# Kernel optimization log

Measured on AMD Instinct MI355X. Metric: run time of the kernel, lower is better.

The kernel has to match this reference:

```python
import jax, jax.numpy as jnp
import numpy as np

# Model config (matches init_kwargs)
DIM = 2048
INTER = 1408          # moe_inter_dim
E = 16                # n_routed_experts
TOPK = 4              # n_activated_experts
G = 4                 # n_expert_groups
TOPK_G = 2            # n_limited_groups
N_SHARED = 2
SHARED_INTER = N_SHARED * INTER  # 2816
ROUTE_SCALE = 1.0


def setup_inputs() -> dict:
    key = jax.random.key(0)
    ks = jax.random.split(key, 8)
    s = 0.02
    x = jax.random.normal(ks[0], (1, 2048, DIM), dtype=jnp.float32)
    Wg = jax.random.normal(ks[1], (E, DIM), dtype=jnp.float32) * s      # gate weight
    W1 = jax.random.normal(ks[2], (E, INTER, DIM), dtype=jnp.float32) * s  # expert gate proj
    W3 = jax.random.normal(ks[3], (E, INTER, DIM), dtype=jnp.float32) * s  # expert up proj
    W2 = jax.random.normal(ks[4], (E, DIM, INTER), dtype=jnp.float32) * s  # expert down proj
    Ws1 = jax.random.normal(ks[5], (SHARED_INTER, DIM), dtype=jnp.float32) * s
    Ws3 = jax.random.normal(ks[6], (SHARED_INTER, DIM), dtype=jnp.float32) * s
    Ws2 = jax.random.normal(ks[7], (DIM, SHARED_INTER), dtype=jnp.float32) * s
    return {"x": x, "Wg": Wg, "W1": W1, "W3": W3, "W2": W2,
            "Ws1": Ws1, "Ws3": Ws3, "Ws2": Ws2}


def _moe_forward(x, Wg, W1, W3, W2, Ws1, Ws3, Ws2):
    B, S, D = x.shape
    xt = x.reshape(-1, D)              # [T, D]
    T = xt.shape[0]

    # ---- Gate: group-limited top-k routing (bias is None since dim != 7168) ----
    scores = jax.nn.softmax(xt @ Wg.T, axis=-1)          # [T, E]
    sg = scores.reshape(T, G, E // G)                    # [T, G, E/G]
    group_scores = sg.max(axis=-1)                       # amax per group
    gidx = jax.lax.top_k(group_scores, TOPK_G)[1]        # [T, TOPK_G]
    gmask = jax.nn.one_hot(gidx, G, dtype=jnp.float32).sum(axis=1) > 0  # [T, G] kept groups
    masked = jnp.where(gmask[:, :, None], sg, -jnp.inf).reshape(T, E)
    topi = jax.lax.top_k(masked, TOPK)[1]                # [T, TOPK] expert indices
    weights = jnp.take_along_axis(scores, topi, axis=1) * ROUTE_SCALE  # original_scores gather

    # ---- Routed experts: dense per-expert SwiGLU FFN, zero-weight combine ----
    # combine[t, e] = sum over k of weights[t, k] * (topi[t, k] == e)
    combine = jnp.zeros((T, E), xt.dtype).at[jnp.arange(T)[:, None], topi].add(weights)
    h = jax.nn.silu(jnp.einsum('td,eid->eti', xt, W1)) * jnp.einsum('td,eid->eti', xt, W3)
    expert_out = jnp.einsum('eti,edi->etd', h, W2)       # [E, T, D]
    y = jnp.einsum('etd,te->td', expert_out, combine)    # [T, D]

    # ---- Shared expert (applied to all tokens) ----
    z = (jax.nn.silu(xt @ Ws1.T) * (xt @ Ws3.T)) @ Ws2.T

    return (y + z).reshape(B, S, D)


def reference(x, Wg, W1, W3, W2, Ws1, Ws3, Ws2):
    return _moe_forward(x, Wg, W1, W3, W2, Ws1, Ws3, Ws2)
```

## Files before the change

kernel.cpp:

```cpp
#include <hip/hip_runtime.h>
#include <stdint.h>

#define D_MODEL  2048
#define N_INTER  1408
#define SH_INTER 2816
#define T_TOK    2048
#define NSLOT    (T_TOK * 4)

typedef __attribute__((ext_vector_type(8))) short bf16x8;
typedef __attribute__((ext_vector_type(4))) float f32x4;

__device__ __forceinline__ unsigned short f2bf(float f){
  unsigned int b = __builtin_bit_cast(unsigned int, f);
  b = (b + 0x7FFFu + ((b >> 16) & 1u)) >> 16;
  return (unsigned short)b;
}
__device__ __forceinline__ float bf2f(unsigned short h){
  unsigned int b = ((unsigned int)h) << 16;
  return __builtin_bit_cast(float, b);
}

#define GLOAD16(gp, lp) __builtin_amdgcn_global_load_lds( \
    (const __attribute__((address_space(1))) unsigned int*)(gp), \
    (__attribute__((address_space(3))) unsigned int*)(lp), 16, 0, 0)

__global__ void cvt_bf16_kernel(const float* __restrict__ x,
                                unsigned short* __restrict__ o, int n4){
  const int stride = gridDim.x * blockDim.x;
  for (int i = blockIdx.x * blockDim.x + threadIdx.x; i < n4; i += stride){
    const float4 v = ((const float4*)x)[i];
    ushort4 u; u.x = f2bf(v.x); u.y = f2bf(v.y); u.z = f2bf(v.z); u.w = f2bf(v.w);
    ((ushort4*)o)[i] = u;
  }
}

__global__ void gate_kernel(const float* __restrict__ x, const float* __restrict__ Wg,
                            int* __restrict__ cnt, int* __restrict__ list,
                            float* __restrict__ wslot){
  const int t = blockIdx.x;
  const int l = threadIdx.x;
  const int e = l & 15, q = l >> 4;
  const float* xr = x + (size_t)t * D_MODEL + q * 512;
  const float* wr = Wg + (size_t)e * D_MODEL + q * 512;
  float p = 0.f;
  #pragma unroll 4
  for (int i = 0; i < 512; i += 4){
    float4 xv = *(const float4*)(xr + i);
    float4 wv = *(const float4*)(wr + i);
    p += xv.x*wv.x + xv.y*wv.y + xv.z*wv.z + xv.w*wv.w;
  }
  p += __shfl_xor(p, 16);
  p += __shfl_xor(p, 32);
  float mx = p;
  for (int d = 1; d < 16; d <<= 1) mx = fmaxf(mx, __shfl_xor(mx, d));
  float ex = __expf(p - mx);
  float sum = ex;
  for (int d = 1; d < 16; d <<= 1) sum += __shfl_xor(sum, d);
  const float sc = ex / sum;
  float gm = fmaxf(sc, __shfl_xor(sc, 1));
  gm = fmaxf(gm, __shfl_xor(gm, 2));
  const float g0 = __shfl(gm, 0), g1 = __shfl(gm, 4),
              g2 = __shfl(gm, 8), g3 = __shfl(gm, 12);
  const int grp = e >> 2;
  const float gs[4] = {g0, g1, g2, g3};
  int grank = 0;
  #pragma unroll
  for (int j = 0; j < 4; ++j)
    if (gs[j] > gm || (gs[j] == gm && j < grp)) grank++;
  const float msc = (grank < 2) ? sc : -INFINITY;
  int erank = 0;
  #pragma unroll
  for (int j = 0; j < 16; ++j){
    const float oj = __shfl(msc, j);
    if (oj > msc || (oj == msc && j < e)) erank++;
  }
  if (q == 0 && erank < 4 && msc > -INFINITY){
    const int pos = atomicAdd(&cnt[e], 1);
    const int slot = (t << 2) | erank;
    list[e * T_TOK + pos] = slot;
    wslot[slot] = sc;
  }
}

template<int MODE>
__global__ __launch_bounds__(256, 2)
void gemm4_kernel(const unsigned short* __restrict__ A,
                  const unsigned short* __restrict__ B,
                  void* __restrict__ OutP,
                  const int* __restrict__ list,
                  const int* __restrict__ cnt,
                  int N, int K, int MT, int NT)
{
  constexpr bool GATHER = (MODE >= 2);
  __shared__ unsigned short As[2 * 128 * 32];
  __shared__ unsigned short Bs[2 * 128 * 32];

  const int per = gridDim.x >> 3;
  const int gsw = (blockIdx.x & 7) * per + (blockIdx.x >> 3);
  const int mt   = gsw % MT;
  const int rest = gsw / MT;
  const int nt = GATHER ? (rest % NT) : rest;
  const int e  = GATHER ? (rest / NT) : 0;

  const int cntE = GATHER ? cnt[e] : (MT * 128);
  if (mt * 128 >= cntE) return;

  const int tid = threadIdx.x, wid = tid >> 6, lane = tid & 63;

  const int rt0 = 32 * wid + (lane >> 2), rt1 = rt0 + 16;
  const int sx0 = ((lane & 3) ^ ((rt0 >> 1) & 3)) << 3;
  const int sx1 = ((lane & 3) ^ ((rt1 >> 1) & 3)) << 3;

  int ar0, ar1;
  if constexpr (GATHER){
    const int lim = cntE - 1;
    int p0 = mt * 128 + rt0; p0 = p0 < lim ? p0 : lim;
    int p1 = mt * 128 + rt1; p1 = p1 < lim ? p1 : lim;
    const int e0 = list[e * T_TOK + p0], e1 = list[e * T_TOK + p1];
    ar0 = (MODE == 2) ? (e0 >> 2) : e0;
    ar1 = (MODE == 2) ? (e1 >> 2) : e1;
  } else { ar0 = mt * 128 + rt0; ar1 = mt * 128 + rt1; }

  const unsigned short* pa0 = A + (size_t)ar0 * K + sx0;
  const unsigned short* pa1 = A + (size_t)ar1 * K + sx1;
  const size_t Boff = GATHER ? (size_t)e * N * K : 0;
  const unsigned short* pb0 = B + Boff + (size_t)(nt * 128 + rt0) * K + sx0;
  const unsigned short* pb1 = B + Boff + (size_t)(nt * 128 + rt1) * K + sx1;

  const int aW0 = (32 * wid) * 32, aW1 = (32 * wid + 16) * 32;
  const int bufStride = 128 * 32;

  const int wr = wid >> 1, wc = wid & 1, lr = lane & 15, lq = lane >> 4;
  const int fx = ((lq ^ ((lr >> 1) & 3)) << 3);
  int aoff[4], boff[4];
  #pragma unroll
  for (int m = 0; m < 4; ++m) aoff[m] = (wr * 64 + m * 16 + lr) * 32 + fx;
  #pragma unroll
  for (int n = 0; n < 4; ++n) boff[n] = (wc * 64 + n * 16 + lr) * 32 + fx;

  f32x4 acc[4][4];
  const f32x4 zero = {0.f, 0.f, 0.f, 0.f};
  #pragma unroll
  for (int m = 0; m < 4; ++m)
    #pragma unroll
    for (int n = 0; n < 4; ++n) acc[m][n] = zero;

  const int KT = K >> 5;
  GLOAD16(pa0, As + aW0);
  GLOAD16(pa1, As + aW1);
  GLOAD16(pb0, Bs + aW0);
  GLOAD16(pb1, Bs + aW1);
  pa0 += 32; pa1 += 32; pb0 += 32; pb1 += 32;
  int cur = 0;

  for (int kt = 0; kt < KT; ++kt){
    __syncthreads();
    if (kt + 1 < KT){
      const int nx = cur ^ 1;
      GLOAD16(pa0, As + nx * bufStride + aW0);
      GLOAD16(pa1, As + nx * bufStride + aW1);
      GLOAD16(pb0, Bs + nx * bufStride + aW0);
      GLOAD16(pb1, Bs + nx * bufStride + aW1);
      pa0 += 32; pa1 += 32; pb0 += 32; pb1 += 32;
    }
    const unsigned short* aC = As + cur * bufStride;
    const unsigned short* bC = Bs + cur * bufStride;
    bf16x8 af[4];
    #pragma unroll
    for (int m = 0; m < 4; ++m) af[m] = *(const bf16x8*)(aC + aoff[m]);
    #pragma unroll
    for (int n = 0; n < 4; ++n){
      const bf16x8 bfr = *(const bf16x8*)(bC + boff[n]);
      #pragma unroll
      for (int m = 0; m < 4; ++m)
        acc[m][n] = __builtin_amdgcn_mfma_f32_16x16x32_bf16(af[m], bfr, acc[m][n], 0, 0, 0);
    }
    cur ^= 1;
  }

  const int colBase = nt * 128 + wc * 64;
  #pragma unroll
  for (int m = 0; m < 4; ++m){
    #pragma unroll
    for (int r = 0; r < 4; ++r){
      const int grow = mt * 128 + wr * 64 + m * 16 + lq * 4 + r;
      if constexpr (MODE == 1){
        float* op = (float*)OutP + (size_t)grow * N + colBase;
        #pragma unroll
        for (int n = 0; n < 4; ++n) op[n * 16 + lr] = acc[m][n][r];
      } else if constexpr (MODE == 0){
        unsigned short* op = (unsigned short*)OutP + (size_t)grow * N + colBase;
        #pragma unroll
        for (int n = 0; n < 4; ++n) op[n * 16 + lr] = f2bf(acc[m][n][r]);
      } else {
        if (grow >= cntE) continue;
        const int orow = list[e * T_TOK + grow];
        unsigned short* op = (unsigned short*)OutP + (size_t)orow * N + colBase;
        #pragma unroll
        for (int n = 0; n < 4; ++n) op[n * 16 + lr] = f2bf(acc[m][n][r]);
      }
    }
  }
}

__global__ void swiglu_kernel(unsigned short* __restrict__ G,
                              const unsigned short* __restrict__ U, int n8){
  const int stride = gridDim.x * blockDim.x;
  for (int i = blockIdx.x * blockDim.x + threadIdx.x; i < n8; i += stride){
    const bf16x8 g = ((const bf16x8*)G)[i];
    const bf16x8 u = ((const bf16x8*)U)[i];
    bf16x8 h;
    #pragma unroll
    for (int j = 0; j < 8; ++j){
      const float gv = bf2f((unsigned short)g[j]);
      const float uv = bf2f((unsigned short)u[j]);
      h[j] = (short)f2bf(gv / (1.f + __expf(-gv)) * uv);
    }
    ((bf16x8*)G)[i] = h;
  }
}

__global__ void combine_kernel(const unsigned short* __restrict__ H2,
                               const float* __restrict__ wslot,
                               float* __restrict__ out){
  const int t = blockIdx.x;
  const int c = threadIdx.x * 8;
  float w[4];
  #pragma unroll
  for (int k = 0; k < 4; ++k) w[k] = wslot[t * 4 + k];
  float* o = out + (size_t)t * D_MODEL + c;
  float a[8];
  #pragma unroll
  for (int j = 0; j < 8; ++j) a[j] = o[j];
  #pragma unroll
  for (int k = 0; k < 4; ++k){
    const bf16x8 hv = *(const bf16x8*)(H2 + (size_t)(t * 4 + k) * D_MODEL + c);
    #pragma unroll
    for (int j = 0; j < 8; ++j) a[j] += w[k] * bf2f((unsigned short)hv[j]);
  }
  #pragma unroll
  for (int j = 0; j < 8; ++j) o[j] = a[j];
}

extern "C" void kernel_launch(void* const* d_in, const int* in_sizes, int n_in,
                              void* d_out, int out_size, void* d_ws, size_t ws_size,
                              hipStream_t stream)
{
  const float* x   = (const float*)d_in[0];
  const float* Wg  = (const float*)d_in[1];
  const float* W1  = (const float*)d_in[2];
  const float* W3  = (const float*)d_in[3];
  const float* W2  = (const float*)d_in[4];
  const float* Ws1 = (const float*)d_in[5];
  const float* Ws3 = (const float*)d_in[6];
  const float* Ws2 = (const float*)d_in[7];
  float* out = (float*)d_out;

  char* ws = (char*)d_ws;
  int*   cnt   = (int*)(ws);
  int*   list  = (int*)(ws + 4096);
  float* wslot = (float*)(ws + 4096 + 131072);
  unsigned short* xbf  = (unsigned short*)(ws + ((size_t)1   << 20));
  unsigned short* H2   = (unsigned short*)(ws + ((size_t)1   << 20));
  unsigned short* Ubuf = (unsigned short*)(ws + ((size_t)10  << 20));
  unsigned short* Wb   = (unsigned short*)(ws + ((size_t)34  << 20));
  unsigned short* Gbuf = (unsigned short*)(ws + ((size_t)123 << 20));
  unsigned short* Wb2  = Wb + (size_t)SH_INTER * D_MODEL;

  hipMemsetAsync(cnt, 0, 4096, stream);
  cvt_bf16_kernel<<<2048, 256, 0, stream>>>(x, xbf, T_TOK * D_MODEL / 4);
  gate_kernel<<<T_TOK, 64, 0, stream>>>(x, Wg, cnt, list, wslot);

  cvt_bf16_kernel<<<4096, 256, 0, stream>>>(Ws1, Wb,  SH_INTER * D_MODEL / 4);
  cvt_bf16_kernel<<<4096, 256, 0, stream>>>(Ws3, Wb2, SH_INTER * D_MODEL / 4);
  gemm4_kernel<0><<<16 * 22, 256, 0, stream>>>(xbf, Wb,  Gbuf, nullptr, nullptr,
                                               SH_INTER, D_MODEL, 16, 22);
  gemm4_kernel<0><<<16 * 22, 256, 0, stream>>>(xbf, Wb2, Ubuf, nullptr, nullptr,
                                               SH_INTER, D_MODEL, 16, 22);
  swiglu_kernel<<<2048, 256, 0, stream>>>(Gbuf, Ubuf, T_TOK * SH_INTER / 8);
  cvt_bf16_kernel<<<4096, 256, 0, stream>>>(Ws2, Wb, D_MODEL * SH_INTER / 4);
  gemm4_kernel<1><<<16 * 16, 256, 0, stream>>>(Gbuf, Wb, out, nullptr, nullptr,
                                               D_MODEL, SH_INTER, 16, 16);

  cvt_bf16_kernel<<<8192, 256, 0, stream>>>(W1, Wb, 16 * N_INTER * D_MODEL / 4);
  gemm4_kernel<2><<<16 * 11 * 16, 256, 0, stream>>>(xbf, Wb, Gbuf, list, cnt,
                                                    N_INTER, D_MODEL, 16, 11);
  cvt_bf16_kernel<<<8192, 256, 0, stream>>>(W3, Wb, 16 * N_INTER * D_MODEL / 4);
  gemm4_kernel<2><<<16 * 11 * 16, 256, 0, stream>>>(xbf, Wb, Ubuf, list, cnt,
                                                    N_INTER, D_MODEL, 16, 11);
  swiglu_kernel<<<2048, 256, 0, stream>>>(Gbuf, Ubuf, NSLOT * N_INTER / 8);
  cvt_bf16_kernel<<<8192, 256, 0, stream>>>(W2, Wb, 16 * D_MODEL * N_INTER / 4);
  gemm4_kernel<3><<<16 * 16 * 16, 256, 0, stream>>>(Gbuf, Wb, H2, list, cnt,
                                                    D_MODEL, N_INTER, 16, 16);
  combine_kernel<<<T_TOK, 256, 0, stream>>>(H2, wslot, out);
}
```

Before: 670.8 us.

## Fuse fp32 weight conversion into GEMM loads, merge gate/up GEMMs, split-K shared down

Drops the separate fp32-to-bf16 weight conversion passes. The GEMM now loads fp32 weights straight into LDS and converts each fragment to bf16 in registers before the MFMA. The gate and up projections run as one launch over a concatenated N range, with swiglu reading the interleaved output. The shared down-projection uses a 2-way split-K whose partials are summed in the combine kernel. This removes about 4 passes over the weights, but it doubles B-tile LDS traffic and puts conversion ALU work into the inner loop.

Result: slower. 711.6 us (+6.1%).

```diff
diff --git a/kernel.cpp b/kernel.cpp
--- a/kernel.cpp
+++ b/kernel.cpp
@@ -1,4 +1,5 @@
 #include <hip/hip_runtime.h>
+#include <hip/hip_bf16.h>
 #include <stdint.h>
 
 #define D_MODEL  2048
@@ -14,6 +15,10 @@
   unsigned int b = __builtin_bit_cast(unsigned int, f);
   b = (b + 0x7FFFu + ((b >> 16) & 1u)) >> 16;
   return (unsigned short)b;
+}
+__device__ __forceinline__ unsigned short f2bfh(float f){
+  __hip_bfloat16 h = __float2bfloat16(f);
+  return __builtin_bit_cast(unsigned short, h);
 }
 __device__ __forceinline__ float bf2f(unsigned short h){
   unsigned int b = ((unsigned int)h) << 16;
@@ -82,35 +87,43 @@
   }
 }
 
-template<int MODE>
-__global__ __launch_bounds__(256, 2)
-void gemm4_kernel(const unsigned short* __restrict__ A,
-                  const unsigned short* __restrict__ B,
+template<int MODE, int NTH, int KSPLIT>
+__global__ __launch_bounds__(256, 3)
+void gemm5_kernel(const unsigned short* __restrict__ A,
+                  const float* __restrict__ B1,
+                  const float* __restrict__ B3,
                   void* __restrict__ OutP,
                   const int* __restrict__ list,
                   const int* __restrict__ cnt,
-                  int N, int K, int MT, int NT)
+                  int N, int K, int MT, int NTtot, size_t eStride)
 {
   constexpr bool GATHER = (MODE >= 2);
   __shared__ unsigned short As[2 * 128 * 32];
-  __shared__ unsigned short Bs[2 * 128 * 32];
+  __shared__ float          Bs[2 * 128 * 32];
 
   const int per = gridDim.x >> 3;
   const int gsw = (blockIdx.x & 7) * per + (blockIdx.x >> 3);
-  const int mt   = gsw % MT;
-  const int rest = gsw / MT;
-  const int nt = GATHER ? (rest % NT) : rest;
-  const int e  = GATHER ? (rest / NT) : 0;
+  const int mt = gsw % MT;
+  int r1 = gsw / MT;
+  int ks = 0;
+  if constexpr (KSPLIT > 1){ ks = r1 % KSPLIT; r1 /= KSPLIT; }
+  const int nt = GATHER ? (r1 % NTtot) : r1;
+  const int e  = GATHER ? (r1 / NTtot) : 0;
 
   const int cntE = GATHER ? cnt[e] : (MT * 128);
   if (mt * 128 >= cntE) return;
 
+  const float* Bsel; int ntb;
+  if constexpr (NTH > 0){
+    if (nt >= NTH){ Bsel = B3; ntb = nt - NTH; } else { Bsel = B1; ntb = nt; }
+  } else { Bsel = B1; ntb = nt; }
+  if constexpr (GATHER) Bsel += (size_t)e * eStride;
+
   const int tid = threadIdx.x, wid = tid >> 6, lane = tid & 63;
+  const int kOff = ks * (K / KSPLIT);
 
   const int rt0 = 32 * wid + (lane >> 2), rt1 = rt0 + 16;
-  const int sx0 = ((lane & 3) ^ ((rt0 >> 1) & 3)) << 3;
-  const int sx1 = ((lane & 3) ^ ((rt1 >> 1) & 3)) << 3;
-
+  const int sxA = ((lane & 3) ^ ((lane >> 3) & 3)) << 3;
   int ar0, ar1;
   if constexpr (GATHER){
     const int lim = cntE - 1;
@@ -120,23 +133,32 @@
     ar0 = (MODE == 2) ? (e0 >> 2) : e0;
     ar1 = (MODE == 2) ? (e1 >> 2) : e1;
   } else { ar0 = mt * 128 + rt0; ar1 = mt * 128 + rt1; }
-
-  const unsigned short* pa0 = A + (size_t)ar0 * K + sx0;
-  const unsigned short* pa1 = A + (size_t)ar1 * K + sx1;
-  const size_t Boff = GATHER ? (size_t)e * N * K : 0;
-  const unsigned short* pb0 = B + Boff + (size_t)(nt * 128 + rt0) * K + sx0;
-  const unsigned short* pb1 = B + Boff + (size_t)(nt * 128 + rt1) * K + sx1;
-
-  const int aW0 = (32 * wid) * 32, aW1 = (32 * wid + 16) * 32;
-  const int bufStride = 128 * 32;
+  const unsigned short* pa0 = A + (size_t)ar0 * K + kOff + sxA;
+  const unsigned short* pa1 = A + (size_t)ar1 * K + kOff + sxA;
+  const int aW0 = (32 * wid) * 32, aW1 = aW0 + 16 * 32;
+  const int aStride = 128 * 32;
+
+  const int brt = 32 * wid + (lane >> 3);
+  const int sxB = ((lane & 7) ^ ((lane >> 3) & 7)) << 2;
+  const float* pb0 = Bsel + (size_t)(ntb * 128 + brt     ) * K + kOff + sxB;
+  const float* pb1 = Bsel + (size_t)(ntb * 128 + brt +  8) * K + kOff + sxB;
+  const float* pb2 = Bsel + (size_t)(ntb * 128 + brt + 16) * K + kOff + sxB;
+  const float* pb3 = Bsel + (size_t)(ntb * 128 + brt + 24) * K + kOff + sxB;
+  const int bW0 = wid * 1024, bW1 = bW0 + 256, bW2 = bW0 + 512, bW3 = bW0 + 768;
+  const int bStride = 128 * 32;
 
   const int wr = wid >> 1, wc = wid & 1, lr = lane & 15, lq = lane >> 4;
-  const int fx = ((lq ^ ((lr >> 1) & 3)) << 3);
-  int aoff[4], boff[4];
-  #pragma unroll
-  for (int m = 0; m < 4; ++m) aoff[m] = (wr * 64 + m * 16 + lr) * 32 + fx;
-  #pragma unroll
-  for (int n = 0; n < 4; ++n) boff[n] = (wc * 64 + n * 16 + lr) * 32 + fx;
+  const int fxA = ((lq ^ ((lr >> 1) & 3)) << 3);
+  int aoff[4], boff0[4], boff1[4];
+  #pragma unroll
+  for (int m = 0; m < 4; ++m) aoff[m] = (wr * 64 + m * 16 + lr) * 32 + fxA;
+  #pragma unroll
+  for (int n = 0; n < 4; ++n){
+    const int rowB = wc * 64 + n * 16 + lr;
+    const int ph0 = (2 * lq) ^ (lr & 7);
+    boff0[n] = rowB * 32 + ph0 * 4;
+    boff1[n] = rowB * 32 + (ph0 ^ 1) * 4;
+  }
 
   f32x4 acc[4][4];
   const f32x4 zero = {0.f, 0.f, 0.f, 0.f};
@@ -145,32 +167,42 @@
     #pragma unroll
     for (int n = 0; n < 4; ++n) acc[m][n] = zero;
 
-  const int KT = K >> 5;
+  const int KTL = (K >> 5) / KSPLIT;
   GLOAD16(pa0, As + aW0);
   GLOAD16(pa1, As + aW1);
-  GLOAD16(pb0, Bs + aW0);
-  GLOAD16(pb1, Bs + aW1);
-  pa0 += 32; pa1 += 32; pb0 += 32; pb1 += 32;
+  GLOAD16(pb0, Bs + bW0);
+  GLOAD16(pb1, Bs + bW1);
+  GLOAD16(pb2, Bs + bW2);
+  GLOAD16(pb3, Bs + bW3);
+  pa0 += 32; pa1 += 32; pb0 += 32; pb1 += 32; pb2 += 32; pb3 += 32;
   int cur = 0;
 
-  for (int kt = 0; kt < KT; ++kt){
+  for (int kt = 0; kt < KTL; ++kt){
     __syncthreads();
-    if (kt + 1 < KT){
+    if (kt + 1 < KTL){
       const int nx = cur ^ 1;
-      GLOAD16(pa0, As + nx * bufStride + aW0);
-      GLOAD16(pa1, As + nx * bufStride + aW1);
-      GLOAD16(pb0, Bs + nx * bufStride + aW0);
-      GLOAD16(pb1, Bs + nx * bufStride + aW1);
-      pa0 += 32; pa1 += 32; pb0 += 32; pb1 += 32;
+      GLOAD16(pa0, As + nx * aStride + aW0);
+      GLOAD16(pa1, As + nx * aStride + aW1);
+      GLOAD16(pb0, Bs + nx * bStride + bW0);
+      GLOAD16(pb1, Bs + nx * bStride + bW1);
+      GLOAD16(pb2, Bs + nx * bStride + bW2);
+      GLOAD16(pb3, Bs + nx * bStride + bW3);
+      pa0 += 32; pa1 += 32; pb0 += 32; pb1 += 32; pb2 += 32; pb3 += 32;
     }
-    const unsigned short* aC = As + cur * bufStride;
-    const unsigned short* bC = Bs + cur * bufStride;
+    const unsigned short* aC = As + cur * aStride;
+    const float* bC = Bs + cur * bStride;
     bf16x8 af[4];
     #pragma unroll
     for (int m = 0; m < 4; ++m) af[m] = *(const bf16x8*)(aC + aoff[m]);
     #pragma unroll
     for (int n = 0; n < 4; ++n){
-      const bf16x8 bfr = *(const bf16x8*)(bC + boff[n]);
+      const f32x4 v0 = *(const f32x4*)(bC + boff0[n]);
+      const f32x4 v1 = *(const f32x4*)(bC + boff1[n]);
+      bf16x8 bfr;
+      bfr[0] = (short)f2bfh(v0[0]); bfr[1] = (short)f2bfh(v0[1]);
+      bfr[2] = (short)f2bfh(v0[2]); bfr[3] = (short)f2bfh(v0[3]);
+      bfr[4] = (short)f2bfh(v1[0]); bfr[5] = (short)f2bfh(v1[1]);
+      bfr[6] = (short)f2bfh(v1[2]); bfr[7] = (short)f2bfh(v1[3]);
       #pragma unroll
       for (int m = 0; m < 4; ++m)
         acc[m][n] = __builtin_amdgcn_mfma_f32_16x16x32_bf16(af[m], bfr, acc[m][n], 0, 0, 0);
@@ -185,7 +217,7 @@
     for (int r = 0; r < 4; ++r){
       const int grow = mt * 128 + wr * 64 + m * 16 + lq * 4 + r;
       if constexpr (MODE == 1){
-        float* op = (float*)OutP + (size_t)grow * N + colBase;
+        float* op = (float*)OutP + (size_t)ks * MT * 128 * N + (size_t)grow * N + colBase;
         #pragma unroll
         for (int n = 0; n < 4; ++n) op[n * 16 + lr] = acc[m][n][r];
       } else if constexpr (MODE == 0){
@@ -203,12 +235,14 @@
   }
 }
 
-__global__ void swiglu_kernel(unsigned short* __restrict__ G,
-                              const unsigned short* __restrict__ U, int n8){
+__global__ void swiglu_split_kernel(const unsigned short* __restrict__ GU,
+                                    unsigned short* __restrict__ H,
+                                    int n8, int NI8){
   const int stride = gridDim.x * blockDim.x;
   for (int i = blockIdx.x * blockDim.x + threadIdx.x; i < n8; i += stride){
-    const bf16x8 g = ((const bf16x8*)G)[i];
-    const bf16x8 u = ((const bf16x8*)U)[i];
+    const int r = i / NI8, c = i - r * NI8;
+    const bf16x8 g = ((const bf16x8*)GU)[(size_t)r * 2 * NI8 + c];
+    const bf16x8 u = ((const bf16x8*)GU)[(size_t)r * 2 * NI8 + NI8 + c];
     bf16x8 h;
     #pragma unroll
     for (int j = 0; j < 8; ++j){
@@ -216,11 +250,12 @@
       const float uv = bf2f((unsigned short)u[j]);
       h[j] = (short)f2bf(gv / (1.f + __expf(-gv)) * uv);
     }
-    ((bf16x8*)G)[i] = h;
+    ((bf16x8*)H)[i] = h;
   }
 }
 
 __global__ void combine_kernel(const unsigned short* __restrict__ H2,
+                               const float* __restrict__ P,
                                const float* __restrict__ wslot,
                                float* __restrict__ out){
   const int t = blockIdx.x;
@@ -228,16 +263,18 @@
   float w[4];
   #pragma unroll
   for (int k = 0; k < 4; ++k) w[k] = wslot[t * 4 + k];
-  float* o = out + (size_t)t * D_MODEL + c;
+  const float* p0 = P + (size_t)t * D_MODEL + c;
+  const float* p1 = P + (size_t)(T_TOK + t) * D_MODEL + c;
   float a[8];
   #pragma unroll
-  for (int j = 0; j < 8; ++j) a[j] = o[j];
+  for (int j = 0; j < 8; ++j) a[j] = p0[j] + p1[j];
   #pragma unroll
   for (int k = 0; k < 4; ++k){
     const bf16x8 hv = *(const bf16x8*)(H2 + (size_t)(t * 4 + k) * D_MODEL + c);
     #pragma unroll
     for (int j = 0; j < 8; ++j) a[j] += w[k] * bf2f((unsigned short)hv[j]);
   }
+  float* o = out + (size_t)t * D_MODEL + c;
   #pragma unroll
   for (int j = 0; j < 8; ++j) o[j] = a[j];
 }
@@ -261,36 +298,32 @@
   int*   list  = (int*)(ws + 4096);
   float* wslot = (float*)(ws + 4096 + 131072);
   unsigned short* xbf  = (unsigned short*)(ws + ((size_t)1   << 20));
-  unsigned short* H2   = (unsigned short*)(ws + ((size_t)1   << 20));
-  unsigned short* Ubuf = (unsigned short*)(ws + ((size_t)10  << 20));
-  unsigned short* Wb   = (unsigned short*)(ws + ((size_t)34  << 20));
-  unsigned short* Gbuf = (unsigned short*)(ws + ((size_t)123 << 20));
-  unsigned short* Wb2  = Wb + (size_t)SH_INTER * D_MODEL;
+  unsigned short* GU_s = (unsigned short*)(ws + ((size_t)10  << 20));
+  unsigned short* Hs   = (unsigned short*)(ws + ((size_t)34  << 20));
+  unsigned short* GU_r = (unsigned short*)(ws + ((size_t)46  << 20));
+  unsigned short* Hc   = (unsigned short*)(ws + ((size_t)93  << 20));
+  unsigned short* H2   = (unsigned short*)(ws + ((size_t)10  << 20));
+  float*          P    = (float*)        (ws + ((size_t)117 << 20));
 
   hipMemsetAsync(cnt, 0, 4096, stream);
   cvt_bf16_kernel<<<2048, 256, 0, stream>>>(x, xbf, T_TOK * D_MODEL / 4);
   gate_kernel<<<T_TOK, 64, 0, stream>>>(x, Wg, cnt, list, wslot);
 
-  cvt_bf16_kernel<<<4096, 256, 0, stream>>>(Ws1, Wb,  SH_INTER * D_MODEL / 4);
-  cvt_bf16_kernel<<<4096, 256, 0, stream>>>(Ws3, Wb2, SH_INTER * D_MODEL / 4);
-  gemm4_kernel<0><<<16 * 22, 256, 0, stream>>>(xbf, Wb,  Gbuf, nullptr, nullptr,
-                                               SH_INTER, D_MODEL, 16, 22);
-  gemm4_kernel<0><<<16 * 22, 256, 0, stream>>>(xbf, Wb2, Ubuf, nullptr, nullptr,
-                                               SH_INTER, D_MODEL, 16, 22);
-  swiglu_kernel<<<2048, 256, 0, stream>>>(Gbuf, Ubuf, T_TOK * SH_INTER / 8);
-  cvt_bf16_kernel<<<4096, 256, 0, stream>>>(Ws2, Wb, D_MODEL * SH_INTER / 4);
-  gemm4_kernel<1><<<16 * 16, 256, 0, stream>>>(Gbuf, Wb, out, nullptr, nullptr,
-                                               D_MODEL, SH_INTER, 16, 16);
-
-  cvt_bf16_kernel<<<8192, 256, 0, stream>>>(W1, Wb, 16 * N_INTER * D_MODEL / 4);
-  gemm4_kernel<2><<<16 * 11 * 16, 256, 0, stream>>>(xbf, Wb, Gbuf, list, cnt,
-                                                    N_INTER, D_MODEL, 16, 11);
-  cvt_bf16_kernel<<<8192, 256, 0, stream>>>(W3, Wb, 16 * N_INTER * D_MODEL / 4);
-  gemm4_kernel<2><<<16 * 11 * 16, 256, 0, stream>>>(xbf, Wb, Ubuf, list, cnt,
-                                                    N_INTER, D_MODEL, 16, 11);
-  swiglu_kernel<<<2048, 256, 0, stream>>>(Gbuf, Ubuf, NSLOT * N_INTER / 8);
-  cvt_bf16_kernel<<<8192, 256, 0, stream>>>(W2, Wb, 16 * D_MODEL * N_INTER / 4);
-  gemm4_kernel<3><<<16 * 16 * 16, 256, 0, stream>>>(Gbuf, Wb, H2, list, cnt,
-                                                    D_MODEL, N_INTER, 16, 16);
-  combine_kernel<<<T_TOK, 256, 0, stream>>>(H2, wslot, out);
-}
+  gemm5_kernel<0, 22, 1><<<16 * 44, 256, 0, stream>>>(
+      xbf, Ws1, Ws3, GU_s, nullptr, nullptr, 2 * SH_INTER, D_MODEL, 16, 44, 0);
+  swiglu_split_kernel<<<2048, 256, 0, stream>>>(GU_s, Hs, T_TOK * SH_INTER / 8, SH_INTER / 8);
+
+  gemm5_kernel<1, 0, 2><<<16 * 16 * 2, 256, 0, stream>>>(
+      Hs, Ws2, nullptr, P, nullptr, nullptr, D_MODEL, SH_INTER, 16, 16, 0);
+
+  gemm5_kernel<2, 11, 1><<<16 * 22 * 16, 256, 0, stream>>>(
+      xbf, W1, W3, GU_r, list, cnt, 2 * N_INTER, D_MODEL, 16, 22,
+      (size_t)N_INTER * D_MODEL);
+  swiglu_split_kernel<<<2048, 256, 0, stream>>>(GU_r, Hc, NSLOT * N_INTER / 8, N_INTER / 8);
+
+  gemm5_kernel<3, 0, 1><<<16 * 16 * 16, 256, 0, stream>>>(
+      Hc, W2, nullptr, H2, list, cnt, D_MODEL, N_INTER, 16, 16,
+      (size_t)D_MODEL * N_INTER);
+
+  combine_kernel<<<T_TOK, 256, 0, stream>>>(H2, P, wslot, out);
+}
```

## Triple-buffer GEMM pipeline with explicit waitcnt and fuse shared gate/up GEMMs

Applied to the files above, without the earlier changes.

The GEMM goes from double to triple-buffered LDS. It uses explicit vmcnt waits and split barriers so global loads run two tiles ahead of the MFMA work, and occupancy is raised to 3 blocks. The shared-expert gate and up projections are merged into one GEMM over the concatenated weight, with an in-place SwiGLU over the interleaved output. The LDS swizzle is simplified to depend only on the lane, and an A-stride parameter is added. Risks are higher LDS use, register pressure from the 3-block bound, and correctness of the hand-written waitcnt sequencing.

Measured after the change: 604.5 us. 9.9% less time.

```diff
diff --git a/kernel.cpp b/kernel.cpp
--- a/kernel.cpp
+++ b/kernel.cpp
@@ -6,6 +6,7 @@
 #define SH_INTER 2816
 #define T_TOK    2048
 #define NSLOT    (T_TOK * 4)
+#define MIB(x)   ((size_t)(x) << 20)
 
 typedef __attribute__((ext_vector_type(8))) short bf16x8;
 typedef __attribute__((ext_vector_type(4))) float f32x4;
@@ -83,17 +84,17 @@
 }
 
 template<int MODE>
-__global__ __launch_bounds__(256, 2)
-void gemm4_kernel(const unsigned short* __restrict__ A,
+__global__ __launch_bounds__(256, 3)
+void gemm6_kernel(const unsigned short* __restrict__ A,
                   const unsigned short* __restrict__ B,
                   void* __restrict__ OutP,
                   const int* __restrict__ list,
                   const int* __restrict__ cnt,
-                  int N, int K, int MT, int NT)
+                  int N, int K, int Astride, int MT, int NT)
 {
   constexpr bool GATHER = (MODE >= 2);
-  __shared__ unsigned short As[2 * 128 * 32];
-  __shared__ unsigned short Bs[2 * 128 * 32];
+  __shared__ unsigned short As[3 * 128 * 32];
+  __shared__ unsigned short Bs[3 * 128 * 32];
 
   const int per = gridDim.x >> 3;
   const int gsw = (blockIdx.x & 7) * per + (blockIdx.x >> 3);
@@ -108,8 +109,7 @@
   const int tid = threadIdx.x, wid = tid >> 6, lane = tid & 63;
 
   const int rt0 = 32 * wid + (lane >> 2), rt1 = rt0 + 16;
-  const int sx0 = ((lane & 3) ^ ((rt0 >> 1) & 3)) << 3;
-  const int sx1 = ((lane & 3) ^ ((rt1 >> 1) & 3)) << 3;
+  const int sxA = ((lane & 3) ^ ((lane >> 3) & 3)) << 3;
 
   int ar0, ar1;
   if constexpr (GATHER){
@@ -121,13 +121,13 @@
     ar1 = (MODE == 2) ? (e1 >> 2) : e1;
   } else { ar0 = mt * 128 + rt0; ar1 = mt * 128 + rt1; }
 
-  const unsigned short* pa0 = A + (size_t)ar0 * K + sx0;
-  const unsigned short* pa1 = A + (size_t)ar1 * K + sx1;
-  const size_t Boff = GATHER ? (size_t)e * N * K : 0;
-  const unsigned short* pb0 = B + Boff + (size_t)(nt * 128 + rt0) * K + sx0;
-  const unsigned short* pb1 = B + Boff + (size_t)(nt * 128 + rt1) * K + sx1;
-
-  const int aW0 = (32 * wid) * 32, aW1 = (32 * wid + 16) * 32;
+  const unsigned short* pa0 = A + (size_t)ar0 * Astride + sxA;
+  const unsigned short* pa1 = A + (size_t)ar1 * Astride + sxA;
+  const unsigned short* pb0 = B + (GATHER ? (size_t)e * N * K : 0)
+                            + (size_t)(nt * 128 + rt0) * K + sxA;
+  const unsigned short* pb1 = pb0 + (size_t)16 * K;
+
+  const int aW0 = (32 * wid) * 32, aW1 = aW0 + 16 * 32;
   const int bufStride = 128 * 32;
 
   const int wr = wid >> 1, wc = wid & 1, lr = lane & 15, lq = lane >> 4;
@@ -146,36 +146,49 @@
     for (int n = 0; n < 4; ++n) acc[m][n] = zero;
 
   const int KT = K >> 5;
-  GLOAD16(pa0, As + aW0);
-  GLOAD16(pa1, As + aW1);
-  GLOAD16(pb0, Bs + aW0);
-  GLOAD16(pb1, Bs + aW1);
-  pa0 += 32; pa1 += 32; pb0 += 32; pb1 += 32;
-  int cur = 0;
+  #pragma unroll
+  for (int t = 0; t < 3; ++t){
+    GLOAD16(pa0, As + t * bufStride + aW0);
+    GLOAD16(pa1, As + t * bufStride + aW1);
+    GLOAD16(pb0, Bs + t * bufStride + aW0);
+    GLOAD16(pb1, Bs + t * bufStride + aW1);
+    pa0 += 32; pa1 += 32; pb0 += 32; pb1 += 32;
+  }
+  int c = 0;
 
   for (int kt = 0; kt < KT; ++kt){
-    __syncthreads();
-    if (kt + 1 < KT){
-      const int nx = cur ^ 1;
-      GLOAD16(pa0, As + nx * bufStride + aW0);
-      GLOAD16(pa1, As + nx * bufStride + aW1);
-      GLOAD16(pb0, Bs + nx * bufStride + aW0);
-      GLOAD16(pb1, Bs + nx * bufStride + aW1);
+    if (kt < KT - 2)       asm volatile("s_waitcnt vmcnt(8)" ::: "memory");
+    else if (kt == KT - 2) asm volatile("s_waitcnt vmcnt(4)" ::: "memory");
+    else                   asm volatile("s_waitcnt vmcnt(0)" ::: "memory");
+    __builtin_amdgcn_s_barrier();
+
+    const unsigned short* aC = As + c * bufStride;
+    const unsigned short* bC = Bs + c * bufStride;
+    bf16x8 af[4], bf[4];
+    #pragma unroll
+    for (int m = 0; m < 4; ++m) af[m] = *(const bf16x8*)(aC + aoff[m]);
+    #pragma unroll
+    for (int n = 0; n < 4; ++n) bf[n] = *(const bf16x8*)(bC + boff[n]);
+
+    asm volatile("s_waitcnt lgkmcnt(0)" ::: "memory");
+    __builtin_amdgcn_sched_barrier(0);
+    __builtin_amdgcn_s_barrier();
+
+    if (kt + 3 < KT){
+      GLOAD16(pa0, As + c * bufStride + aW0);
+      GLOAD16(pa1, As + c * bufStride + aW1);
+      GLOAD16(pb0, Bs + c * bufStride + aW0);
+      GLOAD16(pb1, Bs + c * bufStride + aW1);
       pa0 += 32; pa1 += 32; pb0 += 32; pb1 += 32;
     }
-    const unsigned short* aC = As + cur * bufStride;
-    const unsigned short* bC = Bs + cur * bufStride;
-    bf16x8 af[4];
-    #pragma unroll
-    for (int m = 0; m < 4; ++m) af[m] = *(const bf16x8*)(aC + aoff[m]);
-    #pragma unroll
-    for (int n = 0; n < 4; ++n){
-      const bf16x8 bfr = *(const bf16x8*)(bC + boff[n]);
+
+    #pragma unroll
+    for (int n = 0; n < 4; ++n)
       #pragma unroll
       for (int m = 0; m < 4; ++m)
-        acc[m][n] = __builtin_amdgcn_mfma_f32_16x16x32_bf16(af[m], bfr, acc[m][n], 0, 0, 0);
-    }
-    cur ^= 1;
+        acc[m][n] = __builtin_amdgcn_mfma_f32_16x16x32_bf16(af[m], bf[n], acc[m][n], 0, 0, 0);
+
+    c = (c == 2) ? 0 : c + 1;
   }
 
   const int colBase = nt * 128 + wc * 64;
@@ -203,8 +216,27 @@
   }
 }
 
-__global__ void swiglu_kernel(unsigned short* __restrict__ G,
-                              const unsigned short* __restrict__ U, int n8){
+__global__ void swiglu_ip_kernel(unsigned short* __restrict__ GU, int n8, int NI8){
+  const int stride = gridDim.x * blockDim.x;
+  bf16x8* p = (bf16x8*)GU;
+  for (int i = blockIdx.x * blockDim.x + threadIdx.x; i < n8; i += stride){
+    const int r = i / NI8, ccol = i - r * NI8;
+    const size_t gi = (size_t)r * 2 * NI8 + ccol;
+    const bf16x8 g = p[gi];
+    const bf16x8 u = p[gi + NI8];
+    bf16x8 h;
+    #pragma unroll
+    for (int j = 0; j < 8; ++j){
+      const float gv = bf2f((unsigned short)g[j]);
+      const float uv = bf2f((unsigned short)u[j]);
+      h[j] = (short)f2bf(gv / (1.f + __expf(-gv)) * uv);
+    }
+    p[gi] = h;
+  }
+}
+
+__global__ void swiglu2_kernel(unsigned short* __restrict__ G,
+                               const unsigned short* __restrict__ U, int n8){
   const int stride = gridDim.x * blockDim.x;
   for (int i = blockIdx.x * blockDim.x + threadIdx.x; i < n8; i += stride){
     const bf16x8 g = ((const bf16x8*)G)[i];
@@ -224,17 +256,17 @@
                                const float* __restrict__ wslot,
                                float* __restrict__ out){
   const int t = blockIdx.x;
-  const int c = threadIdx.x * 8;
+  const int ccol = threadIdx.x * 8;
   float w[4];
   #pragma unroll
   for (int k = 0; k < 4; ++k) w[k] = wslot[t * 4 + k];
-  float* o = out + (size_t)t * D_MODEL + c;
+  float* o = out + (size_t)t * D_MODEL + ccol;
   float a[8];
   #pragma unroll
   for (int j = 0; j < 8; ++j) a[j] = o[j];
   #pragma unroll
   for (int k = 0; k < 4; ++k){
-    const bf16x8 hv = *(const bf16x8*)(H2 + (size_t)(t * 4 + k) * D_MODEL + c);
+    const bf16x8 hv = *(const bf16x8*)(H2 + (size_t)(t * 4 + k) * D_MODEL + ccol);
     #pragma unroll
     for (int j = 0; j < 8; ++j) a[j] += w[k] * bf2f((unsigned short)hv[j]);
   }
@@ -260,11 +292,12 @@
   int*   cnt   = (int*)(ws);
   int*   list  = (int*)(ws + 4096);
   float* wslot = (float*)(ws + 4096 + 131072);
-  unsigned short* xbf  = (unsigned short*)(ws + ((size_t)1   << 20));
-  unsigned short* H2   = (unsigned short*)(ws + ((size_t)1   << 20));
-  unsigned short* Ubuf = (unsigned short*)(ws + ((size_t)10  << 20));
-  unsigned short* Wb   = (unsigned short*)(ws + ((size_t)34  << 20));
-  unsigned short* Gbuf = (unsigned short*)(ws + ((size_t)123 << 20));
+  unsigned short* xbf  = (unsigned short*)(ws + MIB(1));
+  unsigned short* H2   = (unsigned short*)(ws + MIB(1));
+  unsigned short* GU_s = (unsigned short*)(ws + MIB(9));
+  unsigned short* Ubuf = (unsigned short*)(ws + MIB(9));
+  unsigned short* Wb   = (unsigned short*)(ws + MIB(33));
+  unsigned short* Gbuf = (unsigned short*)(ws + MIB(121));
   unsigned short* Wb2  = Wb + (size_t)SH_INTER * D_MODEL;
 
   hipMemsetAsync(cnt, 0, 4096, stream);
@@ -273,24 +306,22 @@
 
   cvt_bf16_kernel<<<4096, 256, 0, stream>>>(Ws1, Wb,  SH_INTER * D_MODEL / 4);
   cvt_bf16_kernel<<<4096, 256, 0, stream>>>(Ws3, Wb2, SH_INTER * D_MODEL / 4);
-  gemm4_kernel<0><<<16 * 22, 256, 0, stream>>>(xbf, Wb,  Gbuf, nullptr, nullptr,
-                                               SH_INTER, D_MODEL, 16, 22);
-  gemm4_kernel<0><<<16 * 22, 256, 0, stream>>>(xbf, Wb2, Ubuf, nullptr, nullptr,
-                                               SH_INTER, D_MODEL, 16, 22);
-  swiglu_kernel<<<2048, 256, 0, stream>>>(Gbuf, Ubuf, T_TOK * SH_INTER / 8);
+  gemm6_kernel<0><<<16 * 44, 256, 0, stream>>>(xbf, Wb, GU_s, nullptr, nullptr,
+                                               2 * SH_INTER, D_MODEL, D_MODEL, 16, 44);
+  swiglu_ip_kernel<<<2048, 256, 0, stream>>>(GU_s, T_TOK * SH_INTER / 8, SH_INTER / 8);
   cvt_bf16_kernel<<<4096, 256, 0, stream>>>(Ws2, Wb, D_MODEL * SH_INTER / 4);
-  gemm4_kernel<1><<<16 * 16, 256, 0, stream>>>(Gbuf, Wb, out, nullptr, nullptr,
-                                               D_MODEL, SH_INTER, 16, 16);
+  gemm6_kernel<1><<<16 * 16, 256, 0, stream>>>(GU_s, Wb, out, nullptr, nullptr,
+                                               D_MODEL, SH_INTER, 2 * SH_INTER, 16, 16);
 
   cvt_bf16_kernel<<<8192, 256, 0, stream>>>(W1, Wb, 16 * N_INTER * D_MODEL / 4);
-  gemm4_kernel<2><<<16 * 11 * 16, 256, 0, stream>>>(xbf, Wb, Gbuf, list, cnt,
-                                                    N_INTER, D_MODEL, 16, 11);
+  gemm6_kernel<2><<<16 * 11 * 16, 256, 0, stream>>>(xbf, Wb, Gbuf, list, cnt,
+                                                    N_INTER, D_MODEL, D_MODEL, 16, 11);
   cvt_bf16_kernel<<<8192, 256, 0, stream>>>(W3, Wb, 16 * N_INTER * D_MODEL / 4);
-  gemm4_kernel<2><<<16 * 11 * 16, 256, 0, stream>>>(xbf, Wb, Ubuf, list, cnt,
-                                                    N_INTER, D_MODEL, 16, 11);
-  swiglu_kernel<<<2048, 256, 0, stream>>>(Gbuf, Ubuf, NSLOT * N_INTER / 8);
+  gemm6_kernel<2><<<16 * 11 * 16, 256, 0, stream>>>(xbf, Wb, Ubuf, list, cnt,
+                                                    N_INTER, D_MODEL, D_MODEL, 16, 11);
+  swiglu2_kernel<<<2048, 256, 0, stream>>>(Gbuf, Ubuf, NSLOT * N_INTER / 8);
   cvt_bf16_kernel<<<8192, 256, 0, stream>>>(W2, Wb, 16 * D_MODEL * N_INTER / 4);
-  gemm4_kernel<3><<<16 * 16 * 16, 256, 0, stream>>>(Gbuf, Wb, H2, list, cnt,
-                                                    D_MODEL, N_INTER, 16, 16);
+  gemm6_kernel<3><<<16 * 16 * 16, 256, 0, stream>>>(Gbuf, Wb, H2, list, cnt,
+                                                    D_MODEL, N_INTER, N_INTER, 16, 16);
   combine_kernel<<<T_TOK, 256, 0, stream>>>(H2, wslot, out);
 }
```
